# Kernel optimization log

Hardware: AMD Instinct MI355X
Metric: run time of the kernel (lower is better)

Reference implementation:

```python
import jax, jax.numpy as jnp
import numpy as np

ENT_TOTAL = 500000
REL_TOTAL = 1000
H = 128
B = 1024
K = 10  # negative_ent + negative_rel
MARGIN = 1.0


def setup_inputs() -> dict:
    key = jax.random.key(0)
    ks = jax.random.split(key, 8)
    return {
        "ent_embeddings": jax.random.normal(ks[0], (ENT_TOTAL, H), dtype=jnp.float32) * 0.05,
        "rel_matrices": jax.random.normal(ks[1], (REL_TOTAL, H * H), dtype=jnp.float32) * 0.05,
        "pos_h": jax.random.randint(ks[2], (B,), 0, ENT_TOTAL, dtype=jnp.int32),
        "pos_t": jax.random.randint(ks[3], (B,), 0, ENT_TOTAL, dtype=jnp.int32),
        "pos_r": jax.random.randint(ks[4], (B,), 0, REL_TOTAL, dtype=jnp.int32),
        "neg_h": jax.random.randint(ks[5], (B * K,), 0, ENT_TOTAL, dtype=jnp.int32),
        "neg_t": jax.random.randint(ks[6], (B * K,), 0, ENT_TOTAL, dtype=jnp.int32),
        "neg_r": jax.random.randint(ks[7], (B * K,), 0, REL_TOTAL, dtype=jnp.int32),
    }


def _calc_score(ent_emb, rel_mat, h_idx, t_idx, r_idx):
    # gather embeddings / relation matrices per example
    h = ent_emb[h_idx]                          # [N, H]
    t = ent_emb[t_idx]                          # [N, H]
    r = rel_mat[r_idx].reshape(-1, H, H)        # [N, H, H]
    # h * (r @ t), then sum over hidden dim -> per-example score [N]
    rt = jnp.einsum('nij,nj->ni', r, t)         # [N, H]
    return jnp.sum(h * rt, axis=-1)             # [N]


def reference(ent_embeddings, rel_matrices, pos_h, pos_t, pos_r, neg_h, neg_t, neg_r):
    p_score = _calc_score(ent_embeddings, rel_matrices, pos_h, pos_t, pos_r)  # [B]
    n_all = _calc_score(ent_embeddings, rel_matrices, neg_h, neg_t, neg_r)    # [B*K]
    # mean over the K negatives per positive (matches reduce_mean over axis 1)
    n_score = jnp.mean(n_all.reshape(B, K), axis=1)                           # [B]
    loss = jnp.sum(jnp.maximum(n_score - p_score + MARGIN, 0.0))
    return loss
```

## Files before the change

kernel.cpp:

```cpp
#include <hip/hip_runtime.h>

#define H 128
#define NPOS 1024
#define KNEG 10
#define NNEG (NPOS * KNEG)
#define NTOT (NPOS + NNEG)
#define NREL 1000
#define MAXL 256

__global__ __launch_bounds__(256) void rescal_rel_kernel(
    const float* __restrict__ ent,
    const float* __restrict__ rel,
    const int* __restrict__ pos_h, const int* __restrict__ pos_t,
    const int* __restrict__ pos_r,
    const int* __restrict__ neg_h, const int* __restrict__ neg_t,
    const int* __restrict__ neg_r,
    float* __restrict__ scores)
{
    const int r   = blockIdx.x;
    const int tid = threadIdx.x;

    __shared__ float sR[H * H];
    __shared__ float sht[4][2][H];
    __shared__ int   list[MAXL];
    __shared__ int   cnt;

    if (tid == 0) cnt = 0;
    __syncthreads();

    {
        const float4* __restrict__ Rg = (const float4*)(rel + (size_t)r * (H * H));
        float4* __restrict__ Rs = (float4*)sR;
#pragma unroll
        for (int m = 0; m < 16; ++m)
            Rs[m * 256 + tid] = Rg[m * 256 + tid];
    }

    for (int n = tid; n < NTOT; n += 256) {
        const int rn = (n < NPOS) ? pos_r[n] : neg_r[n - NPOS];
        if (rn == r) {
            const int p = atomicAdd(&cnt, 1);
            if (p < MAXL) list[p] = n;
        }
    }
    __syncthreads();

    const int m    = cnt < MAXL ? cnt : MAXL;
    const int wave = tid >> 6;
    const int lane = tid & 63;
    const int half = lane >> 5;
    const int jcb  = lane & 31;

    float* __restrict__ hslot = sht[wave][0];
    float* __restrict__ tslot = sht[wave][1];

    int idx = wave;
    float2 ph = make_float2(0.f, 0.f), pt = make_float2(0.f, 0.f);
    if (idx < m) {
        const int n  = list[idx];
        const int hi = (n < NPOS) ? pos_h[n] : neg_h[n - NPOS];
        const int ti = (n < NPOS) ? pos_t[n] : neg_t[n - NPOS];
        ph = ((const float2*)(ent + (size_t)hi * H))[lane];
        pt = ((const float2*)(ent + (size_t)ti * H))[lane];
    }

    while (idx < m) {
        const int n = list[idx];

        ((float2*)hslot)[lane] = ph;
        ((float2*)tslot)[lane] = pt;
        asm volatile("s_waitcnt lgkmcnt(0)" ::: "memory");

        const int nidx = idx + 4;
        if (nidx < m) {
            const int n2 = list[nidx];
            const int hi = (n2 < NPOS) ? pos_h[n2] : neg_h[n2 - NPOS];
            const int ti = (n2 < NPOS) ? pos_t[n2] : neg_t[n2 - NPOS];
            ph = ((const float2*)(ent + (size_t)hi * H))[lane];
            pt = ((const float2*)(ent + (size_t)ti * H))[lane];
        }

        const float4  t4  = *(const float4*)&tslot[4 * jcb];
        const float4* hs4 = (const float4*)&hslot[half * 64];
        const float4* Rr4 = (const float4*)&sR[(size_t)half * 64 * H];

        float acc = 0.f;
#pragma unroll
        for (int kk = 0; kk < 16; ++kk) {
            const float4 h4 = hs4[kk];
#pragma unroll
            for (int d = 0; d < 4; ++d) {
                const float4 r4 = Rr4[(kk * 4 + d) * 32 + jcb];
                const float  hv = (d == 0) ? h4.x : (d == 1) ? h4.y : (d == 2) ? h4.z : h4.w;
                acc += hv * (r4.x * t4.x + r4.y * t4.y + r4.z * t4.z + r4.w * t4.w);
            }
        }

#pragma unroll
        for (int mask = 32; mask > 0; mask >>= 1)
            acc += __shfl_xor(acc, mask, 64);
        if (lane == 0) scores[n] = acc;

        idx = nidx;
    }
}

__global__ __launch_bounds__(1024) void rescal_loss_kernel(
    const float* __restrict__ scores,
    float* __restrict__ out)
{
    const int b = threadIdx.x;
    const float p = scores[b];
    const float* __restrict__ neg = scores + NPOS + b * KNEG;
    float ns = 0.0f;
#pragma unroll
    for (int k = 0; k < KNEG; ++k) ns += neg[k];
    ns *= (1.0f / KNEG);

    float l = fmaxf(ns - p + 1.0f, 0.0f);

#pragma unroll
    for (int off = 32; off > 0; off >>= 1)
        l += __shfl_down(l, off, 64);

    __shared__ float red[16];
    const int wave = b >> 6;
    if ((b & 63) == 0) red[wave] = l;
    __syncthreads();
    if (b == 0) {
        float s = 0.0f;
#pragma unroll
        for (int w = 0; w < 16; ++w) s += red[w];
        out[0] = s;
    }
}

extern "C" void kernel_launch(void* const* d_in, const int* in_sizes, int n_in,
                              void* d_out, int out_size, void* d_ws, size_t ws_size,
                              hipStream_t stream) {
    const float* ent   = (const float*)d_in[0];
    const float* rel   = (const float*)d_in[1];
    const int* pos_h   = (const int*)d_in[2];
    const int* pos_t   = (const int*)d_in[3];
    const int* pos_r   = (const int*)d_in[4];
    const int* neg_h   = (const int*)d_in[5];
    const int* neg_t   = (const int*)d_in[6];
    const int* neg_r   = (const int*)d_in[7];

    float* scores = (float*)d_ws;
    float* out    = (float*)d_out;

    rescal_rel_kernel<<<NREL, 256, 0, stream>>>(
        ent, rel, pos_h, pos_t, pos_r, neg_h, neg_t, neg_r, scores);
    rescal_loss_kernel<<<1, 1024, 0, stream>>>(scores, out);
}
```

Measured before the change: 371.9 us.

## Process two triples per wave to reuse relation-matrix LDS reads; vectorize index scan

Each wave now scores two examples sharing the same relation per iteration, so every float4 of the relation matrix read from LDS feeds two dot products, which roughly halves LDS traffic per example. Entity prefetch is doubled so both pairs are in flight. The relation-index scan now uses int4 loads. The cost is more registers and a wasted half-iteration when a relation has an odd number of examples.

```diff
diff --git a/kernel.cpp b/kernel.cpp
--- a/kernel.cpp
+++ b/kernel.cpp
@@ -21,7 +21,7 @@
     const int tid = threadIdx.x;
 
     __shared__ float sR[H * H];
-    __shared__ float sht[4][2][H];
+    __shared__ float sht[4][4][H];
     __shared__ int   list[MAXL];
     __shared__ int   cnt;
 
@@ -36,11 +36,17 @@
             Rs[m * 256 + tid] = Rg[m * 256 + tid];
     }
 
-    for (int n = tid; n < NTOT; n += 256) {
-        const int rn = (n < NPOS) ? pos_r[n] : neg_r[n - NPOS];
-        if (rn == r) {
-            const int p = atomicAdd(&cnt, 1);
-            if (p < MAXL) list[p] = n;
+    {
+        const int4* __restrict__ pr4 = (const int4*)pos_r;
+        const int4* __restrict__ nr4 = (const int4*)neg_r;
+        for (int q = tid; q < NTOT / 4; q += 256) {
+            int4 v; int base;
+            if (q < NPOS / 4) { v = pr4[q];            base = q * 4; }
+            else              { v = nr4[q - NPOS / 4]; base = NPOS + (q - NPOS / 4) * 4; }
+            if (v.x == r) { int p = atomicAdd(&cnt, 1); if (p < MAXL) list[p] = base + 0; }
+            if (v.y == r) { int p = atomicAdd(&cnt, 1); if (p < MAXL) list[p] = base + 1; }
+            if (v.z == r) { int p = atomicAdd(&cnt, 1); if (p < MAXL) list[p] = base + 2; }
+            if (v.w == r) { int p = atomicAdd(&cnt, 1); if (p < MAXL) list[p] = base + 3; }
         }
     }
     __syncthreads();
@@ -51,57 +57,76 @@
     const int half = lane >> 5;
     const int jcb  = lane & 31;
 
-    float* __restrict__ hslot = sht[wave][0];
-    float* __restrict__ tslot = sht[wave][1];
+    float* __restrict__ h0s = sht[wave][0];
+    float* __restrict__ t0s = sht[wave][1];
+    float* __restrict__ h1s = sht[wave][2];
+    float* __restrict__ t1s = sht[wave][3];
 
-    int idx = wave;
-    float2 ph = make_float2(0.f, 0.f), pt = make_float2(0.f, 0.f);
-    if (idx < m) {
-        const int n  = list[idx];
+    auto fetch = [&](int i, float2& fh, float2& ft) {
+        const int n  = list[i];
         const int hi = (n < NPOS) ? pos_h[n] : neg_h[n - NPOS];
         const int ti = (n < NPOS) ? pos_t[n] : neg_t[n - NPOS];
-        ph = ((const float2*)(ent + (size_t)hi * H))[lane];
-        pt = ((const float2*)(ent + (size_t)ti * H))[lane];
+        fh = ((const float2*)(ent + (size_t)hi * H))[lane];
+        ft = ((const float2*)(ent + (size_t)ti * H))[lane];
+    };
+
+    int p = wave;
+    float2 ph0, pt0, ph1, pt1;
+    if (2 * p < m) {
+        fetch(2 * p, ph0, pt0);
+        fetch((2 * p + 1 < m) ? 2 * p + 1 : 2 * p, ph1, pt1);
     }
 
-    while (idx < m) {
-        const int n = list[idx];
+    while (2 * p < m) {
+        const int  n0   = list[2 * p];
+        const bool has1 = (2 * p + 1 < m);
+        const int  n1   = has1 ? list[2 * p + 1] : n0;
 
-        ((float2*)hslot)[lane] = ph;
-        ((float2*)tslot)[lane] = pt;
+        ((float2*)h0s)[lane] = ph0;
+        ((float2*)t0s)[lane] = pt0;
+        ((float2*)h1s)[lane] = ph1;
+        ((float2*)t1s)[lane] = pt1;
         asm volatile("s_waitcnt lgkmcnt(0)" ::: "memory");
 
-        const int nidx = idx + 4;
-        if (nidx < m) {
-            const int n2 = list[nidx];
-            const int hi = (n2 < NPOS) ? pos_h[n2] : neg_h[n2 - NPOS];
-            const int ti = (n2 < NPOS) ? pos_t[n2] : neg_t[n2 - NPOS];
-            ph = ((const float2*)(ent + (size_t)hi * H))[lane];
-            pt = ((const float2*)(ent + (size_t)ti * H))[lane];
+        const int np = p + 4;
+        if (2 * np < m) {
+            fetch(2 * np, ph0, pt0);
+            fetch((2 * np + 1 < m) ? 2 * np + 1 : 2 * np, ph1, pt1);
         }
 
-        const float4  t4  = *(const float4*)&tslot[4 * jcb];
-        const float4* hs4 = (const float4*)&hslot[half * 64];
-        const float4* Rr4 = (const float4*)&sR[(size_t)half * 64 * H];
+        const float4  t04  = *(const float4*)&t0s[4 * jcb];
+        const float4  t14  = *(const float4*)&t1s[4 * jcb];
+        const float4* h04p = (const float4*)&h0s[half * 64];
+        const float4* h14p = (const float4*)&h1s[half * 64];
+        const float4* Rr4  = (const float4*)&sR[(size_t)half * 64 * H];
 
-        float acc = 0.f;
+        float acc0 = 0.f, acc1 = 0.f;
 #pragma unroll
         for (int kk = 0; kk < 16; ++kk) {
-            const float4 h4 = hs4[kk];
+            const float4 h04 = h04p[kk];
+            const float4 h14 = h14p[kk];
 #pragma unroll
             for (int d = 0; d < 4; ++d) {
                 const float4 r4 = Rr4[(kk * 4 + d) * 32 + jcb];
-                const float  hv = (d == 0) ? h4.x : (d == 1) ? h4.y : (d == 2) ? h4.z : h4.w;
-                acc += hv * (r4.x * t4.x + r4.y * t4.y + r4.z * t4.z + r4.w * t4.w);
+                const float dot0 = r4.x * t04.x + r4.y * t04.y + r4.z * t04.z + r4.w * t04.w;
+                const float dot1 = r4.x * t14.x + r4.y * t14.y + r4.z * t14.z + r4.w * t14.w;
+                const float h0v = (d == 0) ? h04.x : (d == 1) ? h04.y : (d == 2) ? h04.z : h04.w;
+                const float h1v = (d == 0) ? h14.x : (d == 1) ? h14.y : (d == 2) ? h14.z : h14.w;
+                acc0 += h0v * dot0;
+                acc1 += h1v * dot1;
             }
         }
 
 #pragma unroll
-        for (int mask = 32; mask > 0; mask >>= 1)
-            acc += __shfl_xor(acc, mask, 64);
-        if (lane == 0) scores[n] = acc;
-
-        idx = nidx;
+        for (int mask = 32; mask > 0; mask >>= 1) {
+            acc0 += __shfl_xor(acc0, mask, 64);
+            acc1 += __shfl_xor(acc1, mask, 64);
+        }
+        if (lane == 0) {
+            scores[n0] = acc0;
+            if (has1) scores[n1] = acc1;
+        }
+        p = np;
     }
 }
 
```

New measurement: 352.6 us. 1.05x faster.
